# Performance work log

Hardware: AMD Instinct MI355X
Metric: run time of the kernel (lower is better)

The kernel has to match this reference:

```python
import jax, jax.numpy as jnp
import numpy as np

PI = np.pi


def ramp_filter(x):
    """skimage-style ramp filter along the detector axis (axis=2).
    x: [B, C, D, A] sinogram."""
    D = x.shape[2]
    P = max(64, int(2 ** np.ceil(np.log2(2 * D))))  # padded FFT size
    xp = jnp.pad(x, ((0, 0), (0, 0), (0, P - D), (0, 0)))
    # real-space ramp kernel (Kak & Slaney), then FFT -> frequency filter
    n = np.concatenate([np.arange(1, P // 2 + 1, 2), np.arange(P // 2 - 1, 0, -2)])
    f = np.zeros(P, dtype=np.float64)
    f[0] = 0.25
    f[1::2] = -1.0 / (PI * n) ** 2
    fourier_filter = jnp.asarray(2.0 * np.real(np.fft.fft(f)), dtype=jnp.float32)  # [P]
    proj = jnp.fft.fft(xp, axis=2) * fourier_filter[None, None, :, None]
    return jnp.real(jnp.fft.ifft(proj, axis=2))[:, :, :D, :].astype(x.dtype)


def setup_inputs() -> dict:
    key = jax.random.key(0)
    x = jax.random.normal(key, (2, 1, 512, 180), dtype=jnp.float32)  # [B,C,D,A]
    return {"x": x}


def reference(x):
    B, C, D, A = x.shape
    S = D  # circle=True -> in_size == out_size == detector count
    xf = ramp_filter(x)

    lin = jnp.arange(S, dtype=jnp.float32) * 2.0 / (S - 1) - 1.0
    xg = lin[None, :]  # [1,S], varies along columns (image x)
    yg = lin[:, None]  # [S,1], varies along rows  (image y)
    theta = jnp.deg2rad(jnp.arange(A, dtype=jnp.float32))

    # detector coordinate for each (angle, pixel): T = x*cos(th) - y*sin(th), in [-1,1]
    T = xg[None] * jnp.cos(theta)[:, None, None] - yg[None] * jnp.sin(theta)[:, None, None]  # [A,S,S]

    # grid X selects column i_theta exactly (align_corners=True semantics);
    # grid_sample thus reduces to 1-D linear interpolation along the detector axis.
    pix = (T + 1.0) * (D - 1) * 0.5  # pixel coords in [0, D-1] domain
    i0 = jnp.floor(pix)
    w1 = pix - i0
    i0 = i0.astype(jnp.int32)
    i1 = i0 + 1

    xt = jnp.transpose(xf, (0, 1, 3, 2))  # [B,C,A,D]
    a_idx = jnp.arange(A)[:, None, None]  # [A,1,1]

    def gather(idx):
        valid = ((idx >= 0) & (idx <= D - 1)).astype(xf.dtype)  # zero padding
        idxc = jnp.clip(idx, 0, D - 1)
        g = xt[:, :, a_idx, idxc]  # [B,C,A,S,S]
        return g * valid

    contrib = gather(i0) * (1.0 - w1) + gather(i1) * w1  # [B,C,A,S,S]
    reco = jnp.sum(contrib, axis=2)  # [B,C,S,S]

    circle_mask = ((xg ** 2 + yg ** 2) <= 1.0).astype(reco.dtype)  # [S,S]
    reco = reco * circle_mask
    return reco * jnp.float32(PI / (2.0 * A))
```

## Files before the change

kernel.cpp:

```cpp
#include <hip/hip_runtime.h>
#include <hip/hip_fp16.h>
#include <math.h>

#define D_DET 512
#define N_ANG 180
#define S_IMG 512
#define NPIX  (S_IMG * S_IMG)
#define T_MAX 63

typedef _Float16 half2v __attribute__((ext_vector_type(2)));

__device__ __constant__ float kPI = 3.14159265358979323846f;

__device__ __forceinline__ half2v pack_w1(float w) {
    return __builtin_bit_cast(half2v, __builtin_amdgcn_cvt_pkrtz(1.0f, w));
}

__global__ __launch_bounds__(512) void ramp_filter_kernel(
    const float* __restrict__ x, unsigned* __restrict__ xfh) {
    __shared__ float rp[4][640];
    __shared__ float xf[4][D_DET + 1];

    const int blk = blockIdx.x;
    const int bc  = blk / 45;
    const int a0  = (blk % 45) * 4;
    const int d   = threadIdx.x;

    float4 q = *(const float4*)(x + (bc * D_DET + d) * N_ANG + a0);
    rp[0][64 + d] = q.x;
    rp[1][64 + d] = q.y;
    rp[2][64 + d] = q.z;
    rp[3][64 + d] = q.w;
    if (d < 64) {
        #pragma unroll
        for (int r = 0; r < 4; ++r) { rp[r][d] = 0.0f; rp[r][576 + d] = 0.0f; }
    }
    if (d < 4) xf[d][D_DET] = 0.0f;
    __syncthreads();

    constexpr float PI_ = 3.14159265358979323846f;
    #pragma unroll
    for (int r = 0; r < 4; ++r) {
        const float* rm = &rp[r][64 + d];
        float acc = 0.5f * rm[0];
        #pragma unroll
        for (int k = 0; k < (T_MAX + 1) / 2; ++k) {
            const int   t = 2 * k + 1;
            const float h = -2.0f / (PI_ * PI_ * (float)(t * t));
            acc = fmaf(rm[-t] + rm[t], h, acc);
        }
        xf[r][d] = acc;
    }
    __syncthreads();

    #pragma unroll
    for (int r = 0; r < 4; ++r) {
        const float f0 = xf[r][d];
        const float dl = xf[r][d + 1] - f0;
        const unsigned lo = __half_as_ushort(__float2half_rn(f0));
        const unsigned hi = __half_as_ushort(__float2half_rn(dl));
        xfh[((a0 + r) * D_DET + d) * 2 + bc] = (hi << 16) | lo;
    }
}

__global__ __launch_bounds__(512) void backproj_kernel(
    const uint2* __restrict__ xfh, float* __restrict__ out) {
    __shared__ float2 trig[N_ANG];
    __shared__ float2 red[256];
    const int tid = threadIdx.x;
    if (tid < N_ANG) {
        float th = (float)tid * (kPI / 180.0f);
        float s, c;
        sincosf(th, &s, &c);
        trig[tid] = make_float2(c * 255.5f, s * 255.5f);
    }
    __syncthreads();

    const int bi   = blockIdx.x >> 5;
    const int bj   = blockIdx.x & 31;
    const int half = tid >> 8;
    const int sub  = (tid >> 6) & 3;
    const int lane = tid & 63;
    const int px   = tid & 255;
    const int i = (bi << 4) + ((sub >> 1) << 3) + (lane >> 3);
    const int j = (bj << 4) + ((sub & 1) << 3) + (lane & 7);

    const float xP = (float)j * (2.0f / 511.0f) - 1.0f;
    const float yP = (float)i * (2.0f / 511.0f) - 1.0f;
    const float m  = xP * xP + yP * yP;
    const bool inc = (m <= 1.0f);
    const float xS = inc ? xP : 0.0f;
    const float yS = inc ? yP : 0.0f;

    float a0 = 0.0f, a1 = 0.0f;
    if (__any(inc)) {
        const int abeg = half * 90;
        #pragma unroll 6
        for (int a = abeg; a < abeg + 90; ++a) {
            float2 t  = trig[a];
            float pc  = fmaf(xS, t.x, fmaf(yS, -t.y, 255.5f));
            pc        = fmaxf(pc, 0.0f);
            int   fi  = (int)pc;
            float w   = __builtin_amdgcn_fractf(pc);
            half2v hw = pack_w1(w);
            uint2  g  = xfh[(a << 9) + fi];
            a0 = __builtin_amdgcn_fdot2(hw, __builtin_bit_cast(half2v, g.x), a0, false);
            a1 = __builtin_amdgcn_fdot2(hw, __builtin_bit_cast(half2v, g.y), a1, false);
        }
    }

    if (half == 1) red[px] = make_float2(a0, a1);
    __syncthreads();
    if (half == 0) {
        const float2 r = red[px];
        const float msk = inc ? (kPI / (2.0f * (float)N_ANG)) : 0.0f;
        const int p = i * S_IMG + j;
        out[p]        = (a0 + r.x) * msk;
        out[NPIX + p] = (a1 + r.y) * msk;
    }
}

extern "C" void kernel_launch(void* const* d_in, const int* in_sizes, int n_in,
                              void* d_out, int out_size, void* d_ws, size_t ws_size,
                              hipStream_t stream) {
    const float* x   = (const float*)d_in[0];
    float*       out = (float*)d_out;
    unsigned*    xfh = (unsigned*)d_ws;

    ramp_filter_kernel<<<90, 512, 0, stream>>>(x, xfh);
    backproj_kernel<<<1024, 512, 0, stream>>>((const uint2*)xfh, out);
}
```

Measured before the change: 32.78 us.

## Quantize filtered sinogram to 8-bit with per-angle scales

After: 35.34 us. 1.08x slower.

```diff
diff --git a/kernel.cpp b/kernel.cpp
--- a/kernel.cpp
+++ b/kernel.cpp
@@ -8,18 +8,15 @@
 #define NPIX  (S_IMG * S_IMG)
 #define T_MAX 63
 
-typedef _Float16 half2v __attribute__((ext_vector_type(2)));
-
 __device__ __constant__ float kPI = 3.14159265358979323846f;
 
-__device__ __forceinline__ half2v pack_w1(float w) {
-    return __builtin_bit_cast(half2v, __builtin_amdgcn_cvt_pkrtz(1.0f, w));
-}
-
 __global__ __launch_bounds__(512) void ramp_filter_kernel(
-    const float* __restrict__ x, unsigned* __restrict__ xfh) {
+    const float* __restrict__ x, unsigned short* __restrict__ xfb,
+    float* __restrict__ scl) {
     __shared__ float rp[4][640];
     __shared__ float xf[4][D_DET + 1];
+    __shared__ float wredl[8][4];
+    __shared__ float srow[4];
 
     const int blk = blockIdx.x;
     const int bc  = blk / 45;
@@ -53,26 +50,62 @@
     }
     __syncthreads();
 
+    float g0 = fabsf(xf[0][d]);
+    float g1 = fabsf(xf[1][d]);
+    float g2 = fabsf(xf[2][d]);
+    float g3 = fabsf(xf[3][d]);
+    #pragma unroll
+    for (int o = 32; o > 0; o >>= 1) {
+        g0 = fmaxf(g0, __shfl_xor(g0, o, 64));
+        g1 = fmaxf(g1, __shfl_xor(g1, o, 64));
+        g2 = fmaxf(g2, __shfl_xor(g2, o, 64));
+        g3 = fmaxf(g3, __shfl_xor(g3, o, 64));
+    }
+    if ((d & 63) == 0) {
+        const int wv = d >> 6;
+        wredl[wv][0] = g0; wredl[wv][1] = g1;
+        wredl[wv][2] = g2; wredl[wv][3] = g3;
+    }
+    __syncthreads();
+    if (d < 4) {
+        float s = 1e-20f;
+        #pragma unroll
+        for (int wv = 0; wv < 8; ++wv) s = fmaxf(s, wredl[wv][d]);
+        srow[d] = 127.0f / s;
+        scl[(a0 + d) * 2 + bc] = s * (1.0f / 127.0f);
+    }
+    __syncthreads();
+
     #pragma unroll
     for (int r = 0; r < 4; ++r) {
-        const float f0 = xf[r][d];
-        const float dl = xf[r][d + 1] - f0;
-        const unsigned lo = __half_as_ushort(__float2half_rn(f0));
-        const unsigned hi = __half_as_ushort(__float2half_rn(dl));
-        xfh[((a0 + r) * D_DET + d) * 2 + bc] = (hi << 16) | lo;
+        const float qs = srow[r];
+        int q0 = (int)rintf(xf[r][d] * qs) + 128;
+        int q1 = (int)rintf(xf[r][d + 1] * qs) + 128;
+        xfb[((a0 + r) * D_DET + d) * 2 + bc] = (unsigned short)((q1 << 8) | q0);
     }
 }
 
 __global__ __launch_bounds__(512) void backproj_kernel(
-    const uint2* __restrict__ xfh, float* __restrict__ out) {
-    __shared__ float2 trig[N_ANG];
+    const unsigned* __restrict__ xfb, const float* __restrict__ scl,
+    float* __restrict__ out) {
+    __shared__ float4 trig4[N_ANG];
     __shared__ float2 red[256];
+    __shared__ float  sumS[2][2];
     const int tid = threadIdx.x;
     if (tid < N_ANG) {
         float th = (float)tid * (kPI / 180.0f);
         float s, c;
         sincosf(th, &s, &c);
-        trig[tid] = make_float2(c * 255.5f, s * 255.5f);
+        trig4[tid] = make_float4(c * 255.5f, s * 255.5f,
+                                 scl[tid * 2], scl[tid * 2 + 1]);
+    }
+    __syncthreads();
+    if (tid < 4) {
+        const int h = tid >> 1, im = tid & 1;
+        float s = 0.0f;
+        for (int a = h * 90; a < h * 90 + 90; ++a)
+            s += im ? trig4[a].w : trig4[a].z;
+        sumS[h][im] = s * 128.0f;
     }
     __syncthreads();
 
@@ -97,16 +130,23 @@
         const int abeg = half * 90;
         #pragma unroll 6
         for (int a = abeg; a < abeg + 90; ++a) {
-            float2 t  = trig[a];
+            float4 t  = trig4[a];
             float pc  = fmaf(xS, t.x, fmaf(yS, -t.y, 255.5f));
             pc        = fmaxf(pc, 0.0f);
             int   fi  = (int)pc;
             float w   = __builtin_amdgcn_fractf(pc);
-            half2v hw = pack_w1(w);
-            uint2  g  = xfh[(a << 9) + fi];
-            a0 = __builtin_amdgcn_fdot2(hw, __builtin_bit_cast(half2v, g.x), a0, false);
-            a1 = __builtin_amdgcn_fdot2(hw, __builtin_bit_cast(half2v, g.y), a1, false);
+            unsigned g = xfb[(a << 9) + fi];
+            float u0  = (float)(g & 0xffu);
+            float u1  = (float)((g >> 8) & 0xffu);
+            float v0  = (float)((g >> 16) & 0xffu);
+            float v1  = (float)(g >> 24);
+            float l0  = fmaf(w, u1 - u0, u0);
+            float l1  = fmaf(w, v1 - v0, v0);
+            a0 = fmaf(t.z, l0, a0);
+            a1 = fmaf(t.w, l1, a1);
         }
+        a0 -= sumS[half][0];
+        a1 -= sumS[half][1];
     }
 
     if (half == 1) red[px] = make_float2(a0, a1);
@@ -123,10 +163,11 @@
 extern "C" void kernel_launch(void* const* d_in, const int* in_sizes, int n_in,
                               void* d_out, int out_size, void* d_ws, size_t ws_size,
                               hipStream_t stream) {
-    const float* x   = (const float*)d_in[0];
-    float*       out = (float*)d_out;
-    unsigned*    xfh = (unsigned*)d_ws;
+    const float*    x   = (const float*)d_in[0];
+    float*          out = (float*)d_out;
+    unsigned short* xfb = (unsigned short*)d_ws;
+    float*          scl = (float*)((char*)d_ws + 368640);
 
-    ramp_filter_kernel<<<90, 512, 0, stream>>>(x, xfh);
-    backproj_kernel<<<1024, 512, 0, stream>>>((const uint2*)xfh, out);
+    ramp_filter_kernel<<<90, 512, 0, stream>>>(x, xfb, scl);
+    backproj_kernel<<<1024, 512, 0, stream>>>((const unsigned*)xfb, scl, out);
 }
```

## Stage per-block detector windows in LDS for half of the angles

Applied to the files above, without the earlier changes.

Measured after the change: 27.18 us. -17.1%, faster.

```diff
diff --git a/kernel.cpp b/kernel.cpp
--- a/kernel.cpp
+++ b/kernel.cpp
@@ -7,6 +7,7 @@
 #define S_IMG 512
 #define NPIX  (S_IMG * S_IMG)
 #define T_MAX 63
+#define WIN   32
 
 typedef _Float16 half2v __attribute__((ext_vector_type(2)));
 
@@ -65,25 +66,60 @@
 
 __global__ __launch_bounds__(512) void backproj_kernel(
     const uint2* __restrict__ xfh, float* __restrict__ out) {
-    __shared__ float2 trig[N_ANG];
+    __shared__ float4 trig4[N_ANG];
+    __shared__ uint2  win[90 * WIN];
     __shared__ float2 red[256];
+
     const int tid = threadIdx.x;
+    const int bi  = blockIdx.x >> 5;
+    const int bj  = blockIdx.x & 31;
+    const int i0  = bi << 4;
+    const int j0  = bj << 4;
+
     if (tid < N_ANG) {
         float th = (float)tid * (kPI / 180.0f);
         float s, c;
         sincosf(th, &s, &c);
-        trig[tid] = make_float2(c * 255.5f, s * 255.5f);
+        float c5 = c * 255.5f, s5 = s * 255.5f;
+        float bias = 255.5f, dmf = 0.0f;
+        if (tid >= 90) {
+            float x0 = (float)j0 * (2.0f / 511.0f) - 1.0f;
+            float x1 = (float)(j0 + 15) * (2.0f / 511.0f) - 1.0f;
+            float y0 = (float)i0 * (2.0f / 511.0f) - 1.0f;
+            float y1 = (float)(i0 + 15) * (2.0f / 511.0f) - 1.0f;
+            float pmin = 255.5f + fminf(c5 * x0, c5 * x1)
+                                + fminf(-s5 * y0, -s5 * y1);
+            int dmin = (int)floorf(pmin) - 1;
+            dmin = dmin < 0 ? 0 : (dmin > (D_DET - WIN) ? (D_DET - WIN) : dmin);
+            dmin &= ~1;
+            bias = 255.5f - (float)dmin;
+            dmf  = (float)dmin;
+        }
+        trig4[tid] = make_float4(c5, s5, bias, dmf);
     }
     __syncthreads();
 
-    const int bi   = blockIdx.x >> 5;
-    const int bj   = blockIdx.x & 31;
+    {
+        const uint4* __restrict__ src4 = (const uint4*)xfh;
+        uint4* win4 = (uint4*)win;
+        #pragma unroll
+        for (int f = tid; f < 90 * (WIN / 2); f += 512) {
+            int a    = f >> 4;
+            int e    = f & 15;
+            int ag   = 90 + a;
+            int dmin = (int)trig4[ag].w;
+            win4[f]  = src4[((ag << 9) + dmin) >> 1];
+            win4[f]  = src4[(((ag << 9) + dmin) >> 1) + e];
+        }
+    }
+    __syncthreads();
+
     const int half = tid >> 8;
     const int sub  = (tid >> 6) & 3;
     const int lane = tid & 63;
     const int px   = tid & 255;
-    const int i = (bi << 4) + ((sub >> 1) << 3) + (lane >> 3);
-    const int j = (bj << 4) + ((sub & 1) << 3) + (lane & 7);
+    const int i = i0 + ((sub >> 1) << 3) + (lane >> 3);
+    const int j = j0 + ((sub & 1) << 3) + (lane & 7);
 
     const float xP = (float)j * (2.0f / 511.0f) - 1.0f;
     const float yP = (float)i * (2.0f / 511.0f) - 1.0f;
@@ -94,18 +130,32 @@
 
     float a0 = 0.0f, a1 = 0.0f;
     if (__any(inc)) {
-        const int abeg = half * 90;
-        #pragma unroll 6
-        for (int a = abeg; a < abeg + 90; ++a) {
-            float2 t  = trig[a];
-            float pc  = fmaf(xS, t.x, fmaf(yS, -t.y, 255.5f));
-            pc        = fmaxf(pc, 0.0f);
-            int   fi  = (int)pc;
-            float w   = __builtin_amdgcn_fractf(pc);
-            half2v hw = pack_w1(w);
-            uint2  g  = xfh[(a << 9) + fi];
-            a0 = __builtin_amdgcn_fdot2(hw, __builtin_bit_cast(half2v, g.x), a0, false);
-            a1 = __builtin_amdgcn_fdot2(hw, __builtin_bit_cast(half2v, g.y), a1, false);
+        if (half == 0) {
+            #pragma unroll 6
+            for (int a = 0; a < 90; ++a) {
+                float4 t  = trig4[a];
+                float pc  = fmaf(xS, t.x, fmaf(yS, -t.y, 255.5f));
+                pc        = fmaxf(pc, 0.0f);
+                int   fi  = (int)pc;
+                float w   = __builtin_amdgcn_fractf(pc);
+                half2v hw = pack_w1(w);
+                uint2  g  = xfh[(a << 9) + fi];
+                a0 = __builtin_amdgcn_fdot2(hw, __builtin_bit_cast(half2v, g.x), a0, false);
+                a1 = __builtin_amdgcn_fdot2(hw, __builtin_bit_cast(half2v, g.y), a1, false);
+            }
+        } else {
+            #pragma unroll 6
+            for (int a = 90; a < N_ANG; ++a) {
+                float4 t  = trig4[a];
+                float pc  = fmaf(xS, t.x, fmaf(yS, -t.y, t.z));
+                pc        = fminf(fmaxf(pc, 0.0f), (float)(WIN - 1));
+                int   fi  = (int)pc;
+                float w   = __builtin_amdgcn_fractf(pc);
+                half2v hw = pack_w1(w);
+                uint2  g  = win[((a - 90) << 5) + fi];
+                a0 = __builtin_amdgcn_fdot2(hw, __builtin_bit_cast(half2v, g.x), a0, false);
+                a1 = __builtin_amdgcn_fdot2(hw, __builtin_bit_cast(half2v, g.y), a1, false);
+            }
         }
     }
 
```
